# Performance work log

Measured on AMD Instinct MI355X. Metric: run time of the kernel, lower is better.

## Reference

```python
import jax, jax.numpy as jnp
import numpy as np

# Dims: B=2, S=2048, D=1024 hidden, E=8 experts, F=2752 ffn (SwiGLU), top-1 gate,
# capacity_factor=1.0 -> capacity C = (B*S)//E = 512. Residual-MoE (moe_use_residual=True).

def setup_inputs() -> dict:
    key = jax.random.key(0)
    ks = jax.random.split(key, 10)
    B, S, D, E, F = 2, 2048, 1024, 8, 2752
    sc = 0.02
    return {
        "hidden_states": jax.random.normal(ks[0], (B, S, D), jnp.float32),
        "wg":  jax.random.normal(ks[1], (D, E), jnp.float32) * sc,   # gate
        "w1":  jax.random.normal(ks[2], (E, D, F), jnp.float32) * sc,  # expert SwiGLU
        "w3":  jax.random.normal(ks[3], (E, D, F), jnp.float32) * sc,
        "w2":  jax.random.normal(ks[4], (E, F, D), jnp.float32) * sc,
        "rw1": jax.random.normal(ks[5], (D, F), jnp.float32) * sc,    # residual MLP (SwiGLU, no bias)
        "rw3": jax.random.normal(ks[6], (D, F), jnp.float32) * sc,
        "rw2": jax.random.normal(ks[7], (F, D), jnp.float32) * sc,
        "cw":  jax.random.normal(ks[8], (D, 2), jnp.float32) * sc,    # coefficient Linear(D, 2)
        "cb":  jnp.zeros((2,), jnp.float32),
    }


def _moe_forward(x, wg, w1, w3, w2):
    """GShard/DeepSpeed-style top-1 gated MoE with capacity + token dropping.
    x: [T, D] flattened tokens. Returns (out [T,D], l_aux scalar, exp_counts [E])."""
    T, D = x.shape
    E = wg.shape[1]
    C = max(4, T // E)  # capacity_factor = 1.0, min_capacity = 4

    logits = x @ wg                                  # [T, E]
    gates = jax.nn.softmax(logits, axis=-1)
    idx = jnp.argmax(gates, axis=-1)                 # top-1 expert per token
    mask1 = jax.nn.one_hot(idx, E, dtype=gates.dtype)  # [T, E]
    exp_counts = jnp.sum(mask1, axis=0).astype(jnp.int32)

    # load-balancing aux loss (DeepSpeed top1gating)
    me = jnp.mean(gates, axis=0)
    ce = jnp.mean(mask1, axis=0)
    l_aux = jnp.sum(me * ce) * E

    # position of each token within its expert's buffer; drop overflow
    locations = jnp.cumsum(mask1, axis=0) - 1.0      # [T, E]
    mask1 = mask1 * (locations < C)
    loc_s = jnp.sum(locations * mask1, axis=1).astype(jnp.int32)  # [T]
    gates1 = jnp.sum(gates * mask1, axis=1)          # [T] gate weight (0 if dropped)

    loc_oh = jax.nn.one_hot(loc_s, C, dtype=gates.dtype)          # [T, C]
    combine = gates1[:, None, None] * mask1[:, :, None] * loc_oh[:, None, :]  # [T, E, C]
    dispatch = (combine > 0).astype(x.dtype)

    xe = jnp.einsum("tec,td->ecd", dispatch, x)      # dispatch to [E, C, D]
    h = jax.nn.silu(jnp.einsum("ecd,edf->ecf", xe, w1)) * jnp.einsum("ecd,edf->ecf", xe, w3)
    ye = jnp.einsum("ecf,efd->ecd", h, w2)           # expert SwiGLU FFN
    out = jnp.einsum("tec,ecd->td", combine, ye)     # weighted combine back to tokens
    return out, l_aux, exp_counts


def reference(hidden_states, wg, w1, w3, w2, rw1, rw3, rw2, cw, cb):
    B, S, D = hidden_states.shape
    x = hidden_states.reshape(-1, D)
    moe_out, l_aux, exp_counts = _moe_forward(x, wg, w1, w3, w2)
    moe_out = moe_out.reshape(B, S, D)

    # residual SwiGLU MLP + softmax-gated combine (Residual-MoE)
    mlp = (jax.nn.silu(hidden_states @ rw1) * (hidden_states @ rw3)) @ rw2
    coef = jax.nn.softmax(hidden_states @ cw + cb, axis=-1)  # [B, S, 2]
    output = moe_out * coef[..., 0:1] + mlp * coef[..., 1:2]
    return output, l_aux, exp_counts
```

## Files before the change

kernel.cpp:

```cpp
#include <hip/hip_runtime.h>
#include <hip/hip_bf16.h>
#include <stdint.h>

#define T_TOK 4096
#define DD 1024
#define EE 8
#define CC 512
#define FF 2752

typedef __attribute__((ext_vector_type(8))) short bf16x8;
typedef __attribute__((ext_vector_type(4))) float f32x4;
typedef __attribute__((ext_vector_type(4))) unsigned short us4;
typedef __attribute__((ext_vector_type(8))) unsigned short us8;

__device__ __forceinline__ float bf2f(unsigned short u) {
  union { float f; unsigned int i; } v; v.i = ((unsigned int)u) << 16; return v.f;
}
__device__ __forceinline__ unsigned short f2bf(float f) {
  union { float f; unsigned int i; } v; v.f = f;
  unsigned int r = v.i + 0x7fffu + ((v.i >> 16) & 1u);
  return (unsigned short)(r >> 16);
}

#define GLDS16(g, l) __builtin_amdgcn_global_load_lds( \
    (const __attribute__((address_space(1))) void*)(g), \
    (__attribute__((address_space(3))) void*)(l), 16, 0, 0)

#define STG_CHUNK(l) (((l & 3) ^ ((l >> 3) & 3)) * 8)
#define RD_OFF(fr, fq) ((fr) * 32 + (((fq) ^ (((fr) >> 1) & 3)) * 8))

#define BAR() do { asm volatile("" ::: "memory"); __builtin_amdgcn_s_barrier(); \
                   asm volatile("" ::: "memory"); } while (0)

template<int RT>
__global__ __launch_bounds__(256)
void transpose_k(const float* __restrict__ in, const float* __restrict__ in2,
                 unsigned short* __restrict__ out, unsigned short* __restrict__ out2,
                 int R, int C, long inStride, long outStride) {
  __shared__ unsigned short sm[RT * 64];
  int b = blockIdx.z;
  if (b < EE) { in += (long)b * inStride; out += (long)b * outStride; }
  else { in = in2; out = out2; }
  int cb = blockIdx.x * 64, rb = blockIdx.y * RT;
  int t = threadIdx.x;
  int rr = t >> 4, c4 = (t & 15) * 4;
#pragma unroll
  for (int i = 0; i < RT / 16; ++i) {
    int r = rr + i * 16;
    float4 v = *(const float4*)(in + (long)(rb + r) * C + cb + c4);
    us4 o; o.x = f2bf(v.x); o.y = f2bf(v.y); o.z = f2bf(v.z); o.w = f2bf(v.w);
    *(us4*)&sm[r * 64 + (c4 ^ (((r >> 3) & 7) << 3))] = o;
  }
  __syncthreads();
#pragma unroll
  for (int j = 0; j < (64 * (RT / 8)) / 256; ++j) {
    int idx = t + j * 256;
    int g, c;
    if (RT == 128) { g = idx & 15; c = idx >> 4; }
    else           { g = idx & 7;  c = idx >> 3; }
    int r8 = g * 8;
    us8 o;
#pragma unroll
    for (int k = 0; k < 8; ++k) {
      int r = r8 + k;
      o[k] = sm[r * 64 + (c ^ (((r >> 3) & 7) << 3))];
    }
    *(us8*)(out + (long)(cb + c) * R + rb + r8) = o;
  }
}

__global__ void zero_me_k(float* me) { if (threadIdx.x < EE) me[threadIdx.x] = 0.0f; }

__global__ void gate_k(const float* __restrict__ x, const float* __restrict__ wg,
                       const float* __restrict__ cw, const float* __restrict__ cbv,
                       int* __restrict__ idx, float* __restrict__ gatev,
                       float* __restrict__ coef, float* __restrict__ me_sum) {
  int tid = threadIdx.x, lane = tid & 63, wv = tid >> 6;
  int t = blockIdx.x * 4 + wv;
  const float* xr = x + (long)t * DD;
  float acc[EE] = {0,0,0,0,0,0,0,0};
  float c0 = 0.0f, c1 = 0.0f;
  for (int d = lane; d < DD; d += 64) {
    float xv = xr[d];
#pragma unroll
    for (int e = 0; e < EE; ++e) acc[e] += xv * wg[d * EE + e];
    c0 += xv * cw[d * 2 + 0];
    c1 += xv * cw[d * 2 + 1];
  }
#pragma unroll
  for (int o = 32; o > 0; o >>= 1) {
#pragma unroll
    for (int e = 0; e < EE; ++e) acc[e] += __shfl_xor(acc[e], o);
    c0 += __shfl_xor(c0, o);
    c1 += __shfl_xor(c1, o);
  }
  __shared__ float sme[EE];
  if (tid < EE) sme[tid] = 0.0f;
  __syncthreads();
  if (lane == 0) {
    float m = acc[0]; int am = 0;
#pragma unroll
    for (int e = 1; e < EE; ++e) if (acc[e] > m) { m = acc[e]; am = e; }
    float g[EE]; float s = 0.0f;
#pragma unroll
    for (int e = 0; e < EE; ++e) { g[e] = __expf(acc[e] - m); s += g[e]; }
    float inv = 1.0f / s;
    idx[t] = am;
    gatev[t] = g[am] * inv;
#pragma unroll
    for (int e = 0; e < EE; ++e) atomicAdd(&sme[e], g[e] * inv);
    float l0 = c0 + cbv[0], l1 = c1 + cbv[1];
    float mm = fmaxf(l0, l1);
    float e0 = __expf(l0 - mm), e1 = __expf(l1 - mm);
    float is = 1.0f / (e0 + e1);
    coef[t * 2 + 0] = e0 * is;
    coef[t * 2 + 1] = e1 * is;
  }
  __syncthreads();
  if (tid < EE) atomicAdd(&me_sum[tid], sme[tid]);
}

__global__ void scan_k(const int* __restrict__ idx, const float* __restrict__ me_sum,
                       int* __restrict__ slot, int* __restrict__ tok,
                       float* __restrict__ out_tail) {
  __shared__ int sidx[T_TOK];
  __shared__ int counts[EE];
  int tid = threadIdx.x;
  for (int i = tid; i < T_TOK; i += 512) sidx[i] = idx[i];
  __syncthreads();
  int e = tid >> 6, lane = tid & 63;
  int base = 0;
  for (int it = 0; it < T_TOK / 64; ++it) {
    int t = it * 64 + lane;
    bool f = (sidx[t] == e);
    unsigned long long m = __ballot(f);
    if (f) {
      int loc = base + __popcll(m & ((1ull << lane) - 1ull));
      slot[t] = (loc < CC) ? loc : -1;
      if (loc < CC) tok[e * CC + loc] = t;
    }
    base += __popcll(m);
  }
  if (lane == 0) counts[e] = base;
  __syncthreads();
  int filled = min(counts[e], CC);
  for (int c = filled + lane; c < CC; c += 64) tok[e * CC + c] = -1;
  if (tid == 0) {
    float la = 0.0f;
    for (int i = 0; i < EE; ++i) la += me_sum[i] * (float)counts[i];
    la *= (float)EE / ((float)T_TOK * (float)T_TOK);
    out_tail[0] = la;
    for (int i = 0; i < EE; ++i) out_tail[1 + i] = (float)counts[i];
  }
}

__global__ void gather_k(const float* __restrict__ x, const int* __restrict__ tok,
                         unsigned short* __restrict__ xb, unsigned short* __restrict__ xe) {
  int r = blockIdx.x, tid = threadIdx.x;
  int d = tid * 4;
  if (r < T_TOK) {
    float4 v = *(const float4*)(x + (long)r * DD + d);
    us4 o; o.x = f2bf(v.x); o.y = f2bf(v.y); o.z = f2bf(v.z); o.w = f2bf(v.w);
    *(us4*)(xb + (long)r * DD + d) = o;
  } else {
    int s = r - T_TOK;
    int t = tok[s];
    us4 o = {0, 0, 0, 0};
    if (t >= 0) {
      float4 v = *(const float4*)(x + (long)t * DD + d);
      o.x = f2bf(v.x); o.y = f2bf(v.y); o.z = f2bf(v.z); o.w = f2bf(v.w);
    }
    *(us4*)(xe + (long)s * DD + d) = o;
  }
}

__global__ __launch_bounds__(512, 2)
void gemm1_k(const unsigned short* __restrict__ xcat,
             const float* __restrict__ w1, const float* __restrict__ w3,
             const float* __restrict__ rw1, const float* __restrict__ rw3,
             unsigned short* __restrict__ Hcat) {
  int lin = blockIdx.x;
  int work = (lin & 7) * 88 + (lin >> 3);
  int mtile, ntile;
  if (work < 352) {
    int e = work / 44, r = work - e * 44;
    ntile = r >> 1;
    mtile = e * 2 + (r & 1);
  } else {
    int q = work - 352;
    ntile = q >> 4;
    mtile = 16 + (q & 15);
  }
  const unsigned short* A = xcat + (size_t)mtile * 256 * DD;
  const float *B1, *B3;
  if (mtile < 16) { int e = mtile >> 1; B1 = w1 + (size_t)e * DD * FF; B3 = w3 + (size_t)e * DD * FF; }
  else { B1 = rw1; B3 = rw3; }
  unsigned short* H = Hcat + (size_t)mtile * 256 * FF;
  int n0 = ntile * 128;

  __shared__ __align__(16) char Lc[147456];
  const unsigned short* ldsS = (const unsigned short*)Lc;

  int tid = threadIdx.x, l = tid & 63, w = tid >> 6;
  int wm = w >> 2, wn = w & 3;
  int fr = l & 15, fq = l >> 4;
  int srow = l >> 2, soff = STG_CHUNK(l);
  int rdo = RD_OFF(fr, fq);

  const unsigned short* gA0 = A + (size_t)(w * 16 + srow) * DD + soff;
  const unsigned short* gA1 = A + (size_t)((8 + w) * 16 + srow) * DD + soff;
  int lrow = l >> 5;
  int kl0 = 2 * w + lrow;
  int kl1 = 16 + 2 * w + lrow;
  int cs0 = (l & 31) ^ (((kl0 >> 3) & 1) << 2);
  int cs1 = (l & 31) ^ (((kl1 >> 3) & 1) << 2);
  int nn0 = n0 + 4 * cs0; if (nn0 >= FF) nn0 = 0;
  int nn1 = n0 + 4 * cs1; if (nn1 >= FF) nn1 = 0;
  const float* gB1a = B1 + (size_t)kl0 * FF + nn0;
  const float* gB1b = B1 + (size_t)kl1 * FF + nn1;
  const float* gB3a = B3 + (size_t)kl0 * FF + nn0;
  const float* gB3b = B3 + (size_t)kl1 * FF + nn1;

  int cb[2];
#pragma unroll
  for (int ni = 0; ni < 2; ++ni)
    cb[ni] = fq * 4096 + ((((wn * 2 + ni) * 64 + fr * 4)) ^ ((fq & 1) << 6));

#define STG1(bb, hw) do { size_t ka = (size_t)(hw) * 32; size_t kb = ka * FF;   \
    GLDS16(gA0 + ka, Lc + (bb) * 16384 + w * 1024);                             \
    GLDS16(gA1 + ka, Lc + (bb) * 16384 + (8 + w) * 1024);                       \
    GLDS16(gB1a + kb, Lc + 49152 + (bb) * 16384 + w * 1024);                    \
    GLDS16(gB1b + kb, Lc + 49152 + (bb) * 16384 + (8 + w) * 1024);              \
    GLDS16(gB3a + kb, Lc + 98304 + (bb) * 16384 + w * 1024);                    \
    GLDS16(gB3b + kb, Lc + 98304 + (bb) * 16384 + (8 + w) * 1024); } while (0)

  f32x4 acc1[8][2] = {};
  f32x4 acc3[8][2] = {};

  const int HN = 32;
  STG1(0, 0);
  STG1(1, 1);

  for (int h = 0; h < HN; ++h) {
    int buf = h % 3;
    int hw = h + 2; if (hw >= HN) hw -= HN;
    int bufw = (buf + 2) % 3;

    asm volatile("s_waitcnt vmcnt(6)" ::: "memory");
    BAR();
    STG1(bufw, hw);

    const char* Bb1 = Lc + 49152 + buf * 16384;
    const char* Bb3 = Lc + 98304 + buf * 16384;
    bf16x8 af[8];
#pragma unroll
    for (int mi = 0; mi < 8; ++mi)
      af[mi] = *(const bf16x8*)(ldsS + buf * 8192 + (wm * 8 + mi) * 512 + rdo);

    {
      float fb[2][8];
#pragma unroll
      for (int ni = 0; ni < 2; ++ni)
#pragma unroll
        for (int j = 0; j < 8; ++j)
          fb[ni][j] = *(const float*)(Bb1 + cb[ni] + j * 512);
      __builtin_amdgcn_s_setprio(1);
#pragma unroll
      for (int ni = 0; ni < 2; ++ni) {
        union { bf16x8 h; unsigned int u[4]; } bu;
#pragma unroll
        for (int p = 0; p < 4; ++p)
          asm("v_cvt_pk_bf16_f32 %0, %1, %2" : "=v"(bu.u[p]) : "v"(fb[ni][2 * p]), "v"(fb[ni][2 * p + 1]));
#pragma unroll
        for (int mi = 0; mi < 8; ++mi)
          acc1[mi][ni] = __builtin_amdgcn_mfma_f32_16x16x32_bf16(af[mi], bu.h, acc1[mi][ni], 0, 0, 0);
      }
      __builtin_amdgcn_s_setprio(0);
    }
    {
      float fb[2][8];
#pragma unroll
      for (int ni = 0; ni < 2; ++ni)
#pragma unroll
        for (int j = 0; j < 8; ++j)
          fb[ni][j] = *(const float*)(Bb3 + cb[ni] + j * 512);
      __builtin_amdgcn_s_setprio(1);
#pragma unroll
      for (int ni = 0; ni < 2; ++ni) {
        union { bf16x8 h; unsigned int u[4]; } bu;
#pragma unroll
        for (int p = 0; p < 4; ++p)
          asm("v_cvt_pk_bf16_f32 %0, %1, %2" : "=v"(bu.u[p]) : "v"(fb[ni][2 * p]), "v"(fb[ni][2 * p + 1]));
#pragma unroll
        for (int mi = 0; mi < 8; ++mi)
          acc3[mi][ni] = __builtin_amdgcn_mfma_f32_16x16x32_bf16(af[mi], bu.h, acc3[mi][ni], 0, 0, 0);
      }
      __builtin_amdgcn_s_setprio(0);
    }
  }
#undef STG1

#pragma unroll
  for (int mi = 0; mi < 8; ++mi)
#pragma unroll
    for (int ni = 0; ni < 2; ++ni)
#pragma unroll
      for (int r = 0; r < 4; ++r) {
        int gm = wm * 128 + mi * 16 + fq * 4 + r;
        int gn = n0 + (wn * 2 + ni) * 16 + fr;
        if (gn < FF) {
          float v1 = acc1[mi][ni][r], v3 = acc3[mi][ni][r];
          float h = v1 / (1.0f + __expf(-v1)) * v3;
          H[(size_t)gm * FF + gn] = f2bf(h);
        }
      }
}

__global__ __launch_bounds__(512, 2)
void gemm2_k(const unsigned short* __restrict__ Hcat,
             const unsigned short* __restrict__ w2t, const unsigned short* __restrict__ rw2t,
             unsigned short* __restrict__ Ycat) {
  int lin = blockIdx.x;
  int work = (lin & 7) * 32 + (lin >> 3);
  int mtile, ntile;
  if (work < 128) {
    int e = work >> 4, r = work & 15;
    ntile = r >> 1;
    mtile = e * 2 + (r & 1);
  } else {
    int q = work - 128;
    ntile = q >> 4;
    mtile = 16 + (q & 15);
  }
  const unsigned short* A = Hcat + (size_t)mtile * 256 * FF;
  const unsigned short* B = (mtile < 16) ? (w2t + (size_t)(mtile >> 1) * (size_t)DD * FF) : rw2t;
  unsigned short* Y = Ycat + (size_t)mtile * 256 * DD;
  int n0 = ntile * 128;

  __shared__ __align__(16) unsigned short lds[73728];
  char* Lc = (char*)lds;

  int tid = threadIdx.x, l = tid & 63, w = tid >> 6;
  int wm = w >> 1, wn = w & 1;
  int fr = l & 15, fq = l >> 4;
  int srow = l >> 2, soff = STG_CHUNK(l);
  int rdo = RD_OFF(fr, fq);

  const unsigned short* gA0 = A + (size_t)(w * 16 + srow) * FF + soff;
  const unsigned short* gA1 = A + (size_t)((8 + w) * 16 + srow) * FF + soff;
  const unsigned short* gB  = B + (size_t)(n0 + w * 16 + srow) * FF + soff;

#define STG2(bb, kk) do {                                          \
    GLDS16(gA0 + (kk), Lc + (bb) * 16384 + w * 1024);              \
    GLDS16(gA1 + (kk), Lc + (bb) * 16384 + (8 + w) * 1024);        \
    GLDS16(gB  + (kk), Lc + 98304 + (bb) * 8192 + w * 1024); } while (0)

  f32x4 acc[4][4] = {};

  const int HN = 86;
#pragma unroll
  for (int hh = 0; hh < 5; ++hh) STG2(hh, hh * 32);
  asm volatile("s_waitcnt vmcnt(12)" ::: "memory");
  BAR();

  int b = 0;
#pragma unroll 2
  for (int h = 0; h < HN; ++h) {
    int bn = b ? b - 1 : 5;
    int hw = h + 5; if (hw >= HN) hw -= HN;
    int kk = hw * 32;
    bf16x8 af[4], bf[4];

#pragma unroll
    for (int mi = 0; mi < 4; ++mi)
      af[mi] = *(const bf16x8*)(lds + b * 8192 + (wm * 4 + mi) * 512 + rdo);
#pragma unroll
    for (int ni = 0; ni < 4; ++ni)
      bf[ni] = *(const bf16x8*)(lds + 49152 + b * 4096 + (wn * 4 + ni) * 512 + rdo);
    STG2(bn, kk);
    asm volatile("s_waitcnt vmcnt(12)" ::: "memory");
    BAR();
    __builtin_amdgcn_s_setprio(1);
#pragma unroll
    for (int mi = 0; mi < 4; ++mi)
#pragma unroll
      for (int ni = 0; ni < 4; ++ni)
        acc[mi][ni] = __builtin_amdgcn_mfma_f32_16x16x32_bf16(af[mi], bf[ni], acc[mi][ni], 0, 0, 0);
    __builtin_amdgcn_s_setprio(0);
    BAR();

    ++b; if (b == 6) b = 0;
  }
#undef STG2

#pragma unroll
  for (int mi = 0; mi < 4; ++mi)
#pragma unroll
    for (int ni = 0; ni < 4; ++ni)
#pragma unroll
      for (int r = 0; r < 4; ++r) {
        int gm = wm * 64 + mi * 16 + fq * 4 + r;
        int gn = n0 + wn * 64 + ni * 16 + fr;
        Y[(size_t)gm * DD + gn] = f2bf(acc[mi][ni][r]);
      }
}

__global__ void combine_k(const unsigned short* __restrict__ Ye, const unsigned short* __restrict__ Yr,
                          const int* __restrict__ idx, const int* __restrict__ slot,
                          const float* __restrict__ gatev, const float* __restrict__ coef,
                          float* __restrict__ out) {
  int t = blockIdx.x, tid = threadIdx.x;
  int d = tid * 4;
  float c0 = coef[t * 2], c1 = coef[t * 2 + 1];
  int s = slot[t];
  float g = gatev[t] * c0;
  us4 vr = *(const us4*)(Yr + (size_t)t * DD + d);
  float4 o;
  if (s >= 0) {
    us4 ve = *(const us4*)(Ye + ((size_t)idx[t] * CC + s) * DD + d);
    o.x = g * bf2f(ve.x) + c1 * bf2f(vr.x);
    o.y = g * bf2f(ve.y) + c1 * bf2f(vr.y);
    o.z = g * bf2f(ve.z) + c1 * bf2f(vr.z);
    o.w = g * bf2f(ve.w) + c1 * bf2f(vr.w);
  } else {
    o.x = c1 * bf2f(vr.x);
    o.y = c1 * bf2f(vr.y);
    o.z = c1 * bf2f(vr.z);
    o.w = c1 * bf2f(vr.w);
  }
  *(float4*)(out + (size_t)t * DD + d) = o;
}

extern "C" void kernel_launch(void* const* d_in, const int* in_sizes, int n_in,
                              void* d_out, int out_size, void* d_ws, size_t ws_size,
                              hipStream_t stream) {
  const float* x   = (const float*)d_in[0];
  const float* wg  = (const float*)d_in[1];
  const float* w1  = (const float*)d_in[2];
  const float* w3  = (const float*)d_in[3];
  const float* w2  = (const float*)d_in[4];
  const float* rw1 = (const float*)d_in[5];
  const float* rw3 = (const float*)d_in[6];
  const float* rw2 = (const float*)d_in[7];
  const float* cw  = (const float*)d_in[8];
  const float* cbv = (const float*)d_in[9];
  float* out = (float*)d_out;

  char* ws = (char*)d_ws;
  size_t o = 0;
  auto alloc = [&](size_t bytes) -> char* {
    char* p = ws + o; o = (o + bytes + 255) & ~(size_t)255; return p;
  };
  unsigned short* w2t  = (unsigned short*)alloc((size_t)EE * DD * FF * 2);
  unsigned short* rw2t = (unsigned short*)alloc((size_t)DD * FF * 2);
  unsigned short* xe   = (unsigned short*)alloc((size_t)T_TOK * DD * 2);
  unsigned short* xb   = (unsigned short*)alloc((size_t)T_TOK * DD * 2);
  unsigned short* He   = (unsigned short*)alloc((size_t)T_TOK * FF * 2);
  unsigned short* Hr   = (unsigned short*)alloc((size_t)T_TOK * FF * 2);
  unsigned short* Ye   = (unsigned short*)alloc((size_t)T_TOK * DD * 2);
  unsigned short* Yr   = (unsigned short*)alloc((size_t)T_TOK * DD * 2);
  int*   idxp  = (int*)alloc(T_TOK * 4);
  float* gatev = (float*)alloc(T_TOK * 4);
  int*   slotp = (int*)alloc(T_TOK * 4);
  int*   tokp  = (int*)alloc(EE * CC * 4);
  float* coefp = (float*)alloc(T_TOK * 2 * 4);
  float* mep   = (float*)alloc(256);
  if (o > ws_size) return;

  transpose_k<64><<<dim3(16, 43, EE + 1), 256, 0, stream>>>(w2, rw2, w2t, rw2t, FF, DD, (long)FF * DD, (long)DD * FF);

  zero_me_k<<<1, 64, 0, stream>>>(mep);
  gate_k<<<T_TOK / 4, 256, 0, stream>>>(x, wg, cw, cbv, idxp, gatev, coefp, mep);
  scan_k<<<1, 512, 0, stream>>>(idxp, mep, slotp, tokp, out + (size_t)T_TOK * DD);
  gather_k<<<2 * T_TOK, 256, 0, stream>>>(x, tokp, xb, xe);
  gemm1_k<<<704, 512, 0, stream>>>(xe, w1, w3, rw1, rw3, He);
  gemm2_k<<<256, 512, 0, stream>>>(He, w2t, rw2t, Ye);
  combine_k<<<T_TOK, 256, 0, stream>>>(Ye, Yr, idxp, slotp, gatev, coefp, out);
}
```

Baseline: 266.1 us.

## Widen gemm2 N-tile to 256 with a three-stage LDS pipeline

```diff
diff --git a/kernel.cpp b/kernel.cpp
--- a/kernel.cpp
+++ b/kernel.cpp
@@ -321,86 +321,81 @@
              const unsigned short* __restrict__ w2t, const unsigned short* __restrict__ rw2t,
              unsigned short* __restrict__ Ycat) {
   int lin = blockIdx.x;
-  int work = (lin & 7) * 32 + (lin >> 3);
+  int work = (lin & 7) * 16 + (lin >> 3);
   int mtile, ntile;
-  if (work < 128) {
-    int e = work >> 4, r = work & 15;
+  if (work < 64) {
+    int e = work >> 3, r = work & 7;
     ntile = r >> 1;
     mtile = e * 2 + (r & 1);
   } else {
-    int q = work - 128;
+    int q = work - 64;
     ntile = q >> 4;
     mtile = 16 + (q & 15);
   }
   const unsigned short* A = Hcat + (size_t)mtile * 256 * FF;
   const unsigned short* B = (mtile < 16) ? (w2t + (size_t)(mtile >> 1) * (size_t)DD * FF) : rw2t;
   unsigned short* Y = Ycat + (size_t)mtile * 256 * DD;
-  int n0 = ntile * 128;
-
-  __shared__ __align__(16) unsigned short lds[73728];
-  char* Lc = (char*)lds;
+  int n0 = ntile * 256;
+
+  __shared__ __align__(16) char Lc[98304];
 
   int tid = threadIdx.x, l = tid & 63, w = tid >> 6;
   int wm = w >> 1, wn = w & 1;
   int fr = l & 15, fq = l >> 4;
   int srow = l >> 2, soff = STG_CHUNK(l);
-  int rdo = RD_OFF(fr, fq);
+  int rdo2 = RD_OFF(fr, fq) * 2;
 
   const unsigned short* gA0 = A + (size_t)(w * 16 + srow) * FF + soff;
   const unsigned short* gA1 = A + (size_t)((8 + w) * 16 + srow) * FF + soff;
-  const unsigned short* gB  = B + (size_t)(n0 + w * 16 + srow) * FF + soff;
+  const unsigned short* gB0 = B + (size_t)(n0 + w * 16 + srow) * FF + soff;
+  const unsigned short* gB1 = B + (size_t)(n0 + (8 + w) * 16 + srow) * FF + soff;
 
 #define STG2(bb, kk) do {                                          \
     GLDS16(gA0 + (kk), Lc + (bb) * 16384 + w * 1024);              \
     GLDS16(gA1 + (kk), Lc + (bb) * 16384 + (8 + w) * 1024);        \
-    GLDS16(gB  + (kk), Lc + 98304 + (bb) * 8192 + w * 1024); } while (0)
-
-  f32x4 acc[4][4] = {};
+    GLDS16(gB0 + (kk), Lc + 49152 + (bb) * 16384 + w * 1024);     \
+    GLDS16(gB1 + (kk), Lc + 49152 + (bb) * 16384 + (8 + w) * 1024); } while (0)
+
+  f32x4 acc[4][8] = {};
 
   const int HN = 86;
-#pragma unroll
-  for (int hh = 0; hh < 5; ++hh) STG2(hh, hh * 32);
-  asm volatile("s_waitcnt vmcnt(12)" ::: "memory");
-  BAR();
-
-  int b = 0;
-#pragma unroll 2
+  STG2(0, 0);
+  STG2(1, 32);
+
   for (int h = 0; h < HN; ++h) {
-    int bn = b ? b - 1 : 5;
-    int hw = h + 5; if (hw >= HN) hw -= HN;
-    int kk = hw * 32;
-    bf16x8 af[4], bf[4];
-
+    int buf = h % 3;
+    int hw = h + 2; if (hw >= HN) hw -= HN;
+    int bufw = (buf + 2) % 3;
+
+    asm volatile("s_waitcnt vmcnt(4)" ::: "memory");
+    BAR();
+    STG2(bufw, hw * 32);
+
+    bf16x8 af[4], bf[8];
 #pragma unroll
     for (int mi = 0; mi < 4; ++mi)
-      af[mi] = *(const bf16x8*)(lds + b * 8192 + (wm * 4 + mi) * 512 + rdo);
-#pragma unroll
-    for (int ni = 0; ni < 4; ++ni)
-      bf[ni] = *(const bf16x8*)(lds + 49152 + b * 4096 + (wn * 4 + ni) * 512 + rdo);
-    STG2(bn, kk);
-    asm volatile("s_waitcnt vmcnt(12)" ::: "memory");
-    BAR();
+      af[mi] = *(const bf16x8*)(Lc + buf * 16384 + (wm * 4 + mi) * 1024 + rdo2);
+#pragma unroll
+    for (int ni = 0; ni < 8; ++ni)
+      bf[ni] = *(const bf16x8*)(Lc + 49152 + buf * 16384 + (wn * 8 + ni) * 1024 + rdo2);
     __builtin_amdgcn_s_setprio(1);
 #pragma unroll
     for (int mi = 0; mi < 4; ++mi)
 #pragma unroll
-      for (int ni = 0; ni < 4; ++ni)
+      for (int ni = 0; ni < 8; ++ni)
         acc[mi][ni] = __builtin_amdgcn_mfma_f32_16x16x32_bf16(af[mi], bf[ni], acc[mi][ni], 0, 0, 0);
     __builtin_amdgcn_s_setprio(0);
-    BAR();
-
-    ++b; if (b == 6) b = 0;
   }
 #undef STG2
 
 #pragma unroll
   for (int mi = 0; mi < 4; ++mi)
 #pragma unroll
-    for (int ni = 0; ni < 4; ++ni)
+    for (int ni = 0; ni < 8; ++ni)
 #pragma unroll
       for (int r = 0; r < 4; ++r) {
         int gm = wm * 64 + mi * 16 + fq * 4 + r;
-        int gn = n0 + wn * 64 + ni * 16 + fr;
+        int gn = n0 + (wn * 8 + ni) * 16 + fr;
         Y[(size_t)gm * DD + gn] = f2bf(acc[mi][ni][r]);
       }
 }
@@ -474,6 +469,6 @@
   scan_k<<<1, 512, 0, stream>>>(idxp, mep, slotp, tokp, out + (size_t)T_TOK * DD);
   gather_k<<<2 * T_TOK, 256, 0, stream>>>(x, tokp, xb, xe);
   gemm1_k<<<704, 512, 0, stream>>>(xe, w1, w3, rw1, rw3, He);
-  gemm2_k<<<256, 512, 0, stream>>>(He, w2t, rw2t, Ye);
+  gemm2_k<<<128, 512, 0, stream>>>(He, w2t, rw2t, Ye);
   combine_k<<<T_TOK, 256, 0, stream>>>(Ye, Yr, idxp, slotp, gatev, coefp, out);
 }
```

After: 284.9 us. 7.1% more time.
